# Kernel optimization log

Hardware: AMD Instinct MI355X
Metric: run time of the kernel (lower is better)

The kernel has to match this reference:

```python
import jax, jax.numpy as jnp
import numpy as np

T = 256   # time steps
F = 64    # features per step
H = 32    # LSTM hidden size
FORGET_BIAS = 1.0  # TF LSTMCell default


def setup_inputs() -> dict:
    key = jax.random.key(0)
    k1, k2, k3 = jax.random.split(key, 3)
    B = 16384
    x = jax.random.normal(k1, (B, T * F), dtype=jnp.float32)
    W_lstm = jax.random.normal(k2, (F + H, 4 * H), dtype=jnp.float32) * 0.1
    b_lstm = jnp.zeros((4 * H,), dtype=jnp.float32)
    W_dense = jax.random.normal(k3, (H, 1), dtype=jnp.float32) * 0.1
    b_dense = jnp.zeros((1,), dtype=jnp.float32)
    return {"x": x, "W_lstm": W_lstm, "b_lstm": b_lstm,
            "W_dense": W_dense, "b_dense": b_dense}


def reference(x, W_lstm, b_lstm, W_dense, b_dense):
    B = x.shape[0]
    # [B, T*F] -> [T, B, F] for scan over time
    xs = x.reshape(B, T, F).transpose(1, 0, 2)

    def step(carry, x_t):
        c, h = carry
        # TF LSTMCell: concat([inputs, h]) @ kernel + bias, gate order i, j, f, o
        gates = jnp.concatenate([x_t, h], axis=-1) @ W_lstm + b_lstm
        i, j, f, o = jnp.split(gates, 4, axis=-1)
        c_new = c * jax.nn.sigmoid(f + FORGET_BIAS) + jax.nn.sigmoid(i) * jnp.tanh(j)
        h_new = jnp.tanh(c_new) * jax.nn.sigmoid(o)
        return (c_new, h_new), None

    c0 = jnp.zeros((B, H), dtype=x.dtype)
    h0 = jnp.zeros((B, H), dtype=x.dtype)
    (c_T, h_T), _ = jax.lax.scan(step, (c0, h0), xs)

    # dense(1) + ELU on the final hidden state, then flatten like predict()
    out = jax.nn.elu(h_T @ W_dense + b_dense)
    return out.reshape(-1)
```

## Files before the change

### kernel.cpp

```cpp
#include <hip/hip_runtime.h>
#include <stdint.h>

#define T_STEPS 256
#define F_IN 64
#define L2E 1.44269504f

typedef __bf16 bf16x8 __attribute__((ext_vector_type(8)));
typedef float f32x4 __attribute__((ext_vector_type(4)));
typedef uint32_t u32;
typedef uint32_t u32x4 __attribute__((ext_vector_type(4)));

#define GLDS16(gp, lp)                                                         \
    __builtin_amdgcn_global_load_lds(                                          \
        (const __attribute__((address_space(1))) unsigned int*)(gp),           \
        (__attribute__((address_space(3))) unsigned int*)(lp), 16, 0, 0)

static __device__ __forceinline__ u32 pk2(float lo, float hi) {
    unsigned short a = __builtin_bit_cast(unsigned short, (__bf16)lo);
    unsigned short b = __builtin_bit_cast(unsigned short, (__bf16)hi);
    return (u32)a | ((u32)b << 16);
}

__global__ __launch_bounds__(256, 1)
void lstm_fused(const float* __restrict__ x,
                const float* __restrict__ Wl,
                const float* __restrict__ bl,
                const float* __restrict__ Wd,
                const float* __restrict__ bd,
                float* __restrict__ out)
{
    __shared__ __align__(16) float xs[4][4][1024];

    const int lane = threadIdx.x & 63;
    const int wid  = threadIdx.x >> 6;
    const int cl   = lane & 15;
    const int g4   = lane >> 4;
    const int rowBase = blockIdx.x * 64 + wid * 16;

#define GSC(q) (((q) >> 1) == 1 ? -2.0f * L2E : -L2E)

    bf16x8 wfrag[3][8];
#pragma unroll
    for (int kc = 0; kc < 3; ++kc) {
#pragma unroll
        for (int q = 0; q < 8; ++q) {
            bf16x8 v;
#pragma unroll
            for (int j = 0; j < 8; ++j)
                v[j] = (__bf16)(GSC(q) * Wl[(kc * 32 + g4 * 8 + j) * 128 + q * 16 + cl]);
            wfrag[kc][q] = v;
        }
    }

    f32x4 biasf[8];
#pragma unroll
    for (int q = 0; q < 8; ++q) {
#pragma unroll
        for (int r = 0; r < 4; ++r) {
            const int gate = q * 16 + g4 * 4 + r;
            biasf[q][r] = GSC(q) * (bl[gate] + ((q >> 1) == 2 ? 1.0f : 0.0f));
        }
    }
    const float bd0 = bd[0];
    float wdl[4], wdh[4];
#pragma unroll
    for (int r = 0; r < 4; ++r) {
        wdl[r] = Wd[4 * g4 + r];
        wdh[r] = Wd[16 + 4 * g4 + r];
    }

    const float* gbase = x + (size_t)(rowBase + (lane >> 2)) * (size_t)(T_STEPS * F_IN)
                           + (size_t)(((lane & 3) ^ ((lane >> 3) & 3)) * 4);

    asm volatile("s_waitcnt vmcnt(0)" ::: "memory");
    __builtin_amdgcn_sched_barrier(0);

#define STAGE(TT, SP) do {                                                     \
    const float* gp = gbase + (TT) * F_IN;                                     \
    GLDS16(gp,      &xs[wid][SP][0]);                                          \
    GLDS16(gp + 16, &xs[wid][SP][256]);                                        \
    GLDS16(gp + 32, &xs[wid][SP][512]);                                        \
    GLDS16(gp + 48, &xs[wid][SP][768]);                                        \
} while (0)

    STAGE(0, 0);
    STAGE(1, 1);
    STAGE(2, 2);

    const int swz = (cl >> 1) & 3;
    const int c0  = ((g4 & 1) * 2)     ^ swz;
    const int c1  = ((g4 & 1) * 2 + 1) ^ swz;
    const int kA  = (g4 >> 1) * 256 + cl * 16;
    const int kB  = kA + 512;

    const int srcA = cl + 32 * (g4 & 1);
    const int srcB = srcA + 16;
    const int sel  = g4 >> 1;

    f32x4 csl = {0.f, 0.f, 0.f, 0.f};
    f32x4 csh = {0.f, 0.f, 0.f, 0.f};
    f32x4 hlv, hhv;
    u32x4 ahw = {0u, 0u, 0u, 0u};
    f32x4 accx[8];

#define CELL(AI, AJ, AF, AO, CS, HV) do {                                      \
    _Pragma("unroll")                                                          \
    for (int r = 0; r < 4; ++r) {                                              \
        float I  = __builtin_amdgcn_exp2f((AI)[r]);                            \
        float J  = __builtin_amdgcn_exp2f((AJ)[r]);                            \
        float Fv = __builtin_amdgcn_exp2f((AF)[r]);                            \
        float O  = __builtin_amdgcn_exp2f((AO)[r]);                            \
        float t3 = (1.0f + I) * (1.0f + J);                                    \
        float uu = 1.0f + Fv;                                                  \
        float np = __builtin_fmaf(J, 2.0f * L2E, -2.0f * L2E);                 \
        float r1 = __builtin_amdgcn_rcpf(t3 * uu);                             \
        float nm = __builtin_fmaf((CS)[r], t3, np * uu);                       \
        float cp = nm * r1;                                                    \
        float C  = __builtin_amdgcn_exp2f(cp);                                 \
        float r2 = __builtin_amdgcn_rcpf((1.0f + C) * (1.0f + O));             \
        (HV)[r] = (1.0f - C) * r2;                                             \
        (CS)[r] = cp;                                                          \
    }                                                                          \
} while (0)

#define XGATES(SLOT) do {                                                      \
    const float* sl = &xs[wid][SLOT][0];                                       \
    f32x4 xr0 = *(const f32x4*)(sl + kA + c0 * 4);                             \
    f32x4 xr1 = *(const f32x4*)(sl + kA + c1 * 4);                             \
    f32x4 xr2 = *(const f32x4*)(sl + kB + c0 * 4);                             \
    f32x4 xr3 = *(const f32x4*)(sl + kB + c1 * 4);                             \
    bf16x8 ax0, ax1;                                                           \
    _Pragma("unroll")                                                          \
    for (int j = 0; j < 4; ++j) {                                              \
        ax0[j]     = (__bf16)xr0[j];                                           \
        ax0[4 + j] = (__bf16)xr1[j];                                           \
        ax1[j]     = (__bf16)xr2[j];                                           \
        ax1[4 + j] = (__bf16)xr3[j];                                           \
    }                                                                          \
    _Pragma("unroll")                                                          \
    for (int q = 0; q < 8; ++q) {                                              \
        f32x4 a = __builtin_amdgcn_mfma_f32_16x16x32_bf16(wfrag[0][q], ax0, biasf[q], 0, 0, 0); \
        accx[q] = __builtin_amdgcn_mfma_f32_16x16x32_bf16(wfrag[1][q], ax1, a, 0, 0, 0);        \
    }                                                                          \
} while (0)

    asm volatile("s_waitcnt vmcnt(8)" ::: "memory");
    __builtin_amdgcn_sched_barrier(0);
    XGATES(0);

#define STEP(TT) do {                                                          \
         \
    bf16x8 ah = __builtin_bit_cast(bf16x8, ahw);                               \
    f32x4 acc[8];                                                              \
    _Pragma("unroll")                                                          \
    for (int q = 0; q < 8; ++q)                                                \
        acc[q] = __builtin_amdgcn_mfma_f32_16x16x32_bf16(wfrag[2][q], ah, accx[q], 0, 0, 0); \
    CELL(acc[0], acc[2], acc[4], acc[6], csl, hlv);                            \
    CELL(acc[1], acc[3], acc[5], acc[7], csh, hhv);                            \
               \
    u32 W0 = pk2(hlv[0], hlv[1]);                                              \
    u32 W1 = pk2(hlv[2], hlv[3]);                                              \
    u32 W2 = pk2(hhv[0], hhv[1]);                                              \
    u32 W3 = pk2(hhv[2], hhv[3]);                                              \
               \
    int A0 = __shfl((int)W0, srcA, 64), A1 = __shfl((int)W1, srcA, 64);        \
    int A2 = __shfl((int)W2, srcA, 64), A3 = __shfl((int)W3, srcA, 64);        \
    int B0 = __shfl((int)W0, srcB, 64), B1 = __shfl((int)W1, srcB, 64);        \
    int B2 = __shfl((int)W2, srcB, 64), B3 = __shfl((int)W3, srcB, 64);        \
    ahw[0] = (u32)(sel ? A2 : A0);                                             \
    ahw[1] = (u32)(sel ? A3 : A1);                                             \
    ahw[2] = (u32)(sel ? B2 : B0);                                             \
    ahw[3] = (u32)(sel ? B3 : B1);                                             \
           \
    const int tpf = ((TT) + 3 < T_STEPS) ? (TT) + 3 : T_STEPS - 1;             \
    STAGE(tpf, ((TT) + 3) & 3);                                                \
    asm volatile("s_waitcnt vmcnt(8)" ::: "memory");                           \
    __builtin_amdgcn_sched_barrier(0);                                         \
    const int tn = ((TT) + 1 < T_STEPS) ? (TT) + 1 : T_STEPS - 1;              \
    XGATES(tn & 3);                                                            \
} while (0)

    for (int t = 0; t < T_STEPS; t += 4) {
        STEP(t);
        STEP(t + 1);
        STEP(t + 2);
        STEP(t + 3);
    }
#undef STEP
#undef XGATES
#undef CELL
#undef STAGE

    asm volatile("s_waitcnt vmcnt(0)" ::: "memory");

    float v = 0.f;
#pragma unroll
    for (int r = 0; r < 4; ++r) {
        v = __builtin_fmaf(hlv[r], wdl[r], v);
        v = __builtin_fmaf(hhv[r], wdh[r], v);
    }
    v += __shfl_xor(v, 16, 64);
    v += __shfl_xor(v, 32, 64);
    if (lane < 16) {
        float z = v + bd0;
        out[rowBase + lane] = z > 0.f ? z : (__expf(z) - 1.0f);
    }
}

extern "C" void kernel_launch(void* const* d_in, const int* in_sizes, int n_in,
                              void* d_out, int out_size, void* d_ws, size_t ws_size,
                              hipStream_t stream) {
    const float* x  = (const float*)d_in[0];
    const float* Wl = (const float*)d_in[1];
    const float* bl = (const float*)d_in[2];
    const float* Wd = (const float*)d_in[3];
    const float* bd = (const float*)d_in[4];
    float* out = (float*)d_out;

    const int rows = out_size;
    const int grid = (rows + 63) / 64;
    hipLaunchKernelGGL(lstm_fused, dim3(grid), dim3(256), 0, stream,
                       x, Wl, bl, Wd, bd, out);
}
```

Before: 240.1 us.

## Stage x in 4-timestep groups of contiguous 1KB row chunks with double buffering

Replaces the per-timestep prefetch, which loaded one 256-byte row slice per lane across 16 rows, with group staging. Each wave now loads 4 timesteps (1 KB contiguous) of every row with one 16-byte load per lane per row, into an XOR-swizzled LDS buffer. There are two group slots and a vmcnt wait once per 4 steps instead of every step. The aim is more contiguous global access and fewer waits per timestep, at the cost of a shallower prefetch window (one group ahead) and more load instructions issued at once.

```diff
diff --git a/kernel.cpp b/kernel.cpp
--- a/kernel.cpp
+++ b/kernel.cpp
@@ -29,7 +29,7 @@
                 const float* __restrict__ bd,
                 float* __restrict__ out)
 {
-    __shared__ __align__(16) float xs[4][4][1024];
+    __shared__ __align__(16) float xg[4][2][16][256];
 
     const int lane = threadIdx.x & 63;
     const int wid  = threadIdx.x >> 6;
@@ -69,33 +69,30 @@
         wdh[r] = Wd[16 + 4 * g4 + r];
     }
 
-    const float* gbase = x + (size_t)(rowBase + (lane >> 2)) * (size_t)(T_STEPS * F_IN)
-                           + (size_t)(((lane & 3) ^ ((lane >> 3) & 3)) * 4);
+    const char* xbase = (const char*)(x + (size_t)rowBase * (size_t)(T_STEPS * F_IN));
+    int loff[8];
+#pragma unroll
+    for (int k = 0; k < 8; ++k) loff[k] = ((lane ^ k) << 4);
 
     asm volatile("s_waitcnt vmcnt(0)" ::: "memory");
     __builtin_amdgcn_sched_barrier(0);
 
-#define STAGE(TT, SP) do {                                                     \
-    const float* gp = gbase + (TT) * F_IN;                                     \
-    GLDS16(gp,      &xs[wid][SP][0]);                                          \
-    GLDS16(gp + 16, &xs[wid][SP][256]);                                        \
-    GLDS16(gp + 32, &xs[wid][SP][512]);                                        \
-    GLDS16(gp + 48, &xs[wid][SP][768]);                                        \
-} while (0)
-
-    STAGE(0, 0);
-    STAGE(1, 1);
-    STAGE(2, 2);
-
-    const int swz = (cl >> 1) & 3;
-    const int c0  = ((g4 & 1) * 2)     ^ swz;
-    const int c1  = ((g4 & 1) * 2 + 1) ^ swz;
-    const int kA  = (g4 >> 1) * 256 + cl * 16;
-    const int kB  = kA + 512;
+#define STAGE_GROUP(G, SL) do {                                                \
+    _Pragma("unroll")                                                          \
+    for (int r = 0; r < 16; ++r) {                                             \
+        const char* gp = xbase + (size_t)r * (size_t)(T_STEPS * F_IN * 4)      \
+                       + (size_t)(G) * 1024 + loff[r & 7];                     \
+        GLDS16(gp, &xg[wid][SL][r][0]);                                        \
+    }                                                                          \
+} while (0)
+
+    STAGE_GROUP(0, 0);
+    STAGE_GROUP(1, 1);
 
     const int srcA = cl + 32 * (g4 & 1);
     const int srcB = srcA + 16;
     const int sel  = g4 >> 1;
+    const int kswz = cl & 7;
 
     f32x4 csl = {0.f, 0.f, 0.f, 0.f};
     f32x4 csh = {0.f, 0.f, 0.f, 0.f};
@@ -123,12 +120,13 @@
     }                                                                          \
 } while (0)
 
-#define XGATES(SLOT) do {                                                      \
-    const float* sl = &xs[wid][SLOT][0];                                       \
-    f32x4 xr0 = *(const f32x4*)(sl + kA + c0 * 4);                             \
-    f32x4 xr1 = *(const f32x4*)(sl + kA + c1 * 4);                             \
-    f32x4 xr2 = *(const f32x4*)(sl + kB + c0 * 4);                             \
-    f32x4 xr3 = *(const f32x4*)(sl + kB + c1 * 4);                             \
+#define XGATES(TT) do {                                                        \
+    const float* base = &xg[wid][((TT) >> 2) & 1][cl][0];                      \
+    const int c00 = (((TT) & 3) * 16 + 2 * g4) ^ kswz;                         \
+    f32x4 xr0 = *(const f32x4*)(base + (size_t)( c00          ) * 4);          \
+    f32x4 xr1 = *(const f32x4*)(base + (size_t)( c00 ^ 1      ) * 4);          \
+    f32x4 xr2 = *(const f32x4*)(base + (size_t)( c00 ^ 8      ) * 4);          \
+    f32x4 xr3 = *(const f32x4*)(base + (size_t)((c00 ^ 8) ^ 1 ) * 4);          \
     bf16x8 ax0, ax1;                                                           \
     _Pragma("unroll")                                                          \
     for (int j = 0; j < 4; ++j) {                                              \
@@ -144,12 +142,7 @@
     }                                                                          \
 } while (0)
 
-    asm volatile("s_waitcnt vmcnt(8)" ::: "memory");
-    __builtin_amdgcn_sched_barrier(0);
-    XGATES(0);
-
-#define STEP(TT) do {                                                          \
-         \
+#define CHAIN() do {                                                           \
     bf16x8 ah = __builtin_bit_cast(bf16x8, ahw);                               \
     f32x4 acc[8];                                                              \
     _Pragma("unroll")                                                          \
@@ -157,12 +150,10 @@
         acc[q] = __builtin_amdgcn_mfma_f32_16x16x32_bf16(wfrag[2][q], ah, accx[q], 0, 0, 0); \
     CELL(acc[0], acc[2], acc[4], acc[6], csl, hlv);                            \
     CELL(acc[1], acc[3], acc[5], acc[7], csh, hhv);                            \
-               \
     u32 W0 = pk2(hlv[0], hlv[1]);                                              \
     u32 W1 = pk2(hlv[2], hlv[3]);                                              \
     u32 W2 = pk2(hhv[0], hhv[1]);                                              \
     u32 W3 = pk2(hhv[2], hhv[3]);                                              \
-               \
     int A0 = __shfl((int)W0, srcA, 64), A1 = __shfl((int)W1, srcA, 64);        \
     int A2 = __shfl((int)W2, srcA, 64), A3 = __shfl((int)W3, srcA, 64);        \
     int B0 = __shfl((int)W0, srcB, 64), B1 = __shfl((int)W1, srcB, 64);        \
@@ -171,25 +162,32 @@
     ahw[1] = (u32)(sel ? A3 : A1);                                             \
     ahw[2] = (u32)(sel ? B2 : B0);                                             \
     ahw[3] = (u32)(sel ? B3 : B1);                                             \
-           \
-    const int tpf = ((TT) + 3 < T_STEPS) ? (TT) + 3 : T_STEPS - 1;             \
-    STAGE(tpf, ((TT) + 3) & 3);                                                \
-    asm volatile("s_waitcnt vmcnt(8)" ::: "memory");                           \
-    __builtin_amdgcn_sched_barrier(0);                                         \
-    const int tn = ((TT) + 1 < T_STEPS) ? (TT) + 1 : T_STEPS - 1;              \
-    XGATES(tn & 3);                                                            \
-} while (0)
-
-    for (int t = 0; t < T_STEPS; t += 4) {
-        STEP(t);
-        STEP(t + 1);
-        STEP(t + 2);
-        STEP(t + 3);
-    }
-#undef STEP
+} while (0)
+
+    asm volatile("s_waitcnt vmcnt(16)" ::: "memory");
+    __builtin_amdgcn_sched_barrier(0);
+    XGATES(0);
+
+    for (int G = 0; G < 64; ++G) {
+        const int t0 = 4 * G;
+        CHAIN(); XGATES(t0 + 1);
+        CHAIN(); XGATES(t0 + 2);
+        CHAIN(); XGATES(t0 + 3);
+        CHAIN();
+        if (G < 62) {
+            STAGE_GROUP(G + 2, G & 1);
+            asm volatile("s_waitcnt vmcnt(16)" ::: "memory");
+        } else {
+            asm volatile("s_waitcnt vmcnt(0)" ::: "memory");
+        }
+        __builtin_amdgcn_sched_barrier(0);
+        const int tn = (t0 + 4 < T_STEPS) ? t0 + 4 : T_STEPS - 1;
+        XGATES(tn);
+    }
+#undef CHAIN
 #undef XGATES
 #undef CELL
-#undef STAGE
+#undef STAGE_GROUP
 
     asm volatile("s_waitcnt vmcnt(0)" ::: "memory");
 
```

Measured after the change: 242.0 us. About the same (+0.8%).

## Halve rows per wave, double grid and occupancy, simplify staging loop

Applied to the files above, without the earlier changes.

Each wave now handles 8 batch rows instead of 16. The grid doubles and launch bounds allow two blocks per CU, which gives more waves to hide the serial recurrence latency. Shared staging shrinks to match, with a new swizzle, and the x-gate MFMAs are folded into the per-step chain with an un-unrolled loop. It also adds an s_sleep stagger for alternating groups of blocks. The risk is that half the MFMA rows are now padding (16x16 tiles with 8 real rows) and each step carries a longer MFMA dependency.

```diff
diff --git a/kernel.cpp b/kernel.cpp
--- a/kernel.cpp
+++ b/kernel.cpp
@@ -8,7 +8,6 @@
 typedef __bf16 bf16x8 __attribute__((ext_vector_type(8)));
 typedef float f32x4 __attribute__((ext_vector_type(4)));
 typedef uint32_t u32;
-typedef uint32_t u32x4 __attribute__((ext_vector_type(4)));
 
 #define GLDS16(gp, lp)                                                         \
     __builtin_amdgcn_global_load_lds(                                          \
@@ -21,7 +20,7 @@
     return (u32)a | ((u32)b << 16);
 }
 
-__global__ __launch_bounds__(256, 1)
+__global__ __launch_bounds__(256, 2)
 void lstm_fused(const float* __restrict__ x,
                 const float* __restrict__ Wl,
                 const float* __restrict__ bl,
@@ -29,13 +28,13 @@
                 const float* __restrict__ bd,
                 float* __restrict__ out)
 {
-    __shared__ __align__(16) float xs[4][4][1024];
+    __shared__ __align__(16) float xs[4][4][512];
 
     const int lane = threadIdx.x & 63;
     const int wid  = threadIdx.x >> 6;
     const int cl   = lane & 15;
     const int g4   = lane >> 4;
-    const int rowBase = blockIdx.x * 64 + wid * 16;
+    const int rowBase = blockIdx.x * 32 + wid * 8;
 
 #define GSC(q) (((q) >> 1) == 1 ? -2.0f * L2E : -L2E)
 
@@ -61,47 +60,36 @@
             biasf[q][r] = GSC(q) * (bl[gate] + ((q >> 1) == 2 ? 1.0f : 0.0f));
         }
     }
-    const float bd0 = bd[0];
-    float wdl[4], wdh[4];
-#pragma unroll
-    for (int r = 0; r < 4; ++r) {
-        wdl[r] = Wd[4 * g4 + r];
-        wdh[r] = Wd[16 + 4 * g4 + r];
-    }
 
-    const float* gbase = x + (size_t)(rowBase + (lane >> 2)) * (size_t)(T_STEPS * F_IN)
-                           + (size_t)(((lane & 3) ^ ((lane >> 3) & 3)) * 4);
+    const char* xbyte = (const char*)(x + (size_t)(rowBase + (lane >> 3)) * (size_t)(T_STEPS * F_IN))
+                      + (size_t)((((lane & 7) ^ ((lane >> 3) & 7)) << 4));
+
+    if ((blockIdx.x >> 8) & 1) __builtin_amdgcn_s_sleep(14);
 
     asm volatile("s_waitcnt vmcnt(0)" ::: "memory");
     __builtin_amdgcn_sched_barrier(0);
 
 #define STAGE(TT, SP) do {                                                     \
-    const float* gp = gbase + (TT) * F_IN;                                     \
-    GLDS16(gp,      &xs[wid][SP][0]);                                          \
-    GLDS16(gp + 16, &xs[wid][SP][256]);                                        \
-    GLDS16(gp + 32, &xs[wid][SP][512]);                                        \
-    GLDS16(gp + 48, &xs[wid][SP][768]);                                        \
+    const char* gp = xbyte + (size_t)(TT) * 256;                               \
+    GLDS16(gp,       &xs[wid][SP][0]);                                         \
+    GLDS16(gp + 128, &xs[wid][SP][256]);                                       \
 } while (0)
 
     STAGE(0, 0);
     STAGE(1, 1);
     STAGE(2, 2);
 
-    const int swz = (cl >> 1) & 3;
-    const int c0  = ((g4 & 1) * 2)     ^ swz;
-    const int c1  = ((g4 & 1) * 2 + 1) ^ swz;
-    const int kA  = (g4 >> 1) * 256 + cl * 16;
-    const int kB  = kA + 512;
-
     const int srcA = cl + 32 * (g4 & 1);
     const int srcB = srcA + 16;
     const int sel  = g4 >> 1;
+    const int r7   = cl & 7;
+    const int offA = r7 * 32 + (((2 * g4) ^ r7) << 2);
 
     f32x4 csl = {0.f, 0.f, 0.f, 0.f};
     f32x4 csh = {0.f, 0.f, 0.f, 0.f};
-    f32x4 hlv, hhv;
-    u32x4 ahw = {0u, 0u, 0u, 0u};
-    f32x4 accx[8];
+    f32x4 hlv = {0.f, 0.f, 0.f, 0.f};
+    f32x4 hhv = {0.f, 0.f, 0.f, 0.f};
+    u32 ahw0 = 0u, ahw1 = 0u, ahw2 = 0u, ahw3 = 0u;
 
 #define CELL(AI, AJ, AF, AO, CS, HV) do {                                      \
     _Pragma("unroll")                                                          \
@@ -123,71 +111,54 @@
     }                                                                          \
 } while (0)
 
-#define XGATES(SLOT) do {                                                      \
-    const float* sl = &xs[wid][SLOT][0];                                       \
-    f32x4 xr0 = *(const f32x4*)(sl + kA + c0 * 4);                             \
-    f32x4 xr1 = *(const f32x4*)(sl + kA + c1 * 4);                             \
-    f32x4 xr2 = *(const f32x4*)(sl + kB + c0 * 4);                             \
-    f32x4 xr3 = *(const f32x4*)(sl + kB + c1 * 4);                             \
-    bf16x8 ax0, ax1;                                                           \
-    _Pragma("unroll")                                                          \
-    for (int j = 0; j < 4; ++j) {                                              \
-        ax0[j]     = (__bf16)xr0[j];                                           \
-        ax0[4 + j] = (__bf16)xr1[j];                                           \
-        ax1[j]     = (__bf16)xr2[j];                                           \
-        ax1[4 + j] = (__bf16)xr3[j];                                           \
-    }                                                                          \
-    _Pragma("unroll")                                                          \
-    for (int q = 0; q < 8; ++q) {                                              \
-        f32x4 a = __builtin_amdgcn_mfma_f32_16x16x32_bf16(wfrag[0][q], ax0, biasf[q], 0, 0, 0); \
-        accx[q] = __builtin_amdgcn_mfma_f32_16x16x32_bf16(wfrag[1][q], ax1, a, 0, 0, 0);        \
-    }                                                                          \
-} while (0)
+#pragma unroll 1
+    for (int t = 0; t < T_STEPS; ++t) {
+        const int tpf = (t + 3 < T_STEPS) ? t + 3 : T_STEPS - 1;
+        STAGE(tpf, (t + 3) & 3);
+        asm volatile("s_waitcnt vmcnt(4)" ::: "memory");
+        __builtin_amdgcn_sched_barrier(0);
 
-    asm volatile("s_waitcnt vmcnt(8)" ::: "memory");
-    __builtin_amdgcn_sched_barrier(0);
-    XGATES(0);
+        const float* sl = &xs[wid][t & 3][0];
+        f32x4 xr0 = *(const f32x4*)(sl + offA);
+        f32x4 xr1 = *(const f32x4*)(sl + (offA ^ 4));
+        f32x4 xr2 = *(const f32x4*)(sl + 256 + offA);
+        f32x4 xr3 = *(const f32x4*)(sl + 256 + (offA ^ 4));
+        bf16x8 ax0, ax1;
+#pragma unroll
+        for (int j = 0; j < 4; ++j) {
+            ax0[j]     = (__bf16)xr0[j];
+            ax0[4 + j] = (__bf16)xr1[j];
+            ax1[j]     = (__bf16)xr2[j];
+            ax1[4 + j] = (__bf16)xr3[j];
+        }
 
-#define STEP(TT) do {                                                          \
-         \
-    bf16x8 ah = __builtin_bit_cast(bf16x8, ahw);                               \
-    f32x4 acc[8];                                                              \
-    _Pragma("unroll")                                                          \
-    for (int q = 0; q < 8; ++q)                                                \
-        acc[q] = __builtin_amdgcn_mfma_f32_16x16x32_bf16(wfrag[2][q], ah, accx[q], 0, 0, 0); \
-    CELL(acc[0], acc[2], acc[4], acc[6], csl, hlv);                            \
-    CELL(acc[1], acc[3], acc[5], acc[7], csh, hhv);                            \
-               \
-    u32 W0 = pk2(hlv[0], hlv[1]);                                              \
-    u32 W1 = pk2(hlv[2], hlv[3]);                                              \
-    u32 W2 = pk2(hhv[0], hhv[1]);                                              \
-    u32 W3 = pk2(hhv[2], hhv[3]);                                              \
-               \
-    int A0 = __shfl((int)W0, srcA, 64), A1 = __shfl((int)W1, srcA, 64);        \
-    int A2 = __shfl((int)W2, srcA, 64), A3 = __shfl((int)W3, srcA, 64);        \
-    int B0 = __shfl((int)W0, srcB, 64), B1 = __shfl((int)W1, srcB, 64);        \
-    int B2 = __shfl((int)W2, srcB, 64), B3 = __shfl((int)W3, srcB, 64);        \
-    ahw[0] = (u32)(sel ? A2 : A0);                                             \
-    ahw[1] = (u32)(sel ? A3 : A1);                                             \
-    ahw[2] = (u32)(sel ? B2 : B0);                                             \
-    ahw[3] = (u32)(sel ? B3 : B1);                                             \
-           \
-    const int tpf = ((TT) + 3 < T_STEPS) ? (TT) + 3 : T_STEPS - 1;             \
-    STAGE(tpf, ((TT) + 3) & 3);                                                \
-    asm volatile("s_waitcnt vmcnt(8)" ::: "memory");                           \
-    __builtin_amdgcn_sched_barrier(0);                                         \
-    const int tn = ((TT) + 1 < T_STEPS) ? (TT) + 1 : T_STEPS - 1;              \
-    XGATES(tn & 3);                                                            \
-} while (0)
+        union { u32 w[4]; bf16x8 v; } ahu;
+        ahu.w[0] = ahw0; ahu.w[1] = ahw1; ahu.w[2] = ahw2; ahu.w[3] = ahw3;
+        bf16x8 ah = ahu.v;
 
-    for (int t = 0; t < T_STEPS; t += 4) {
-        STEP(t);
-        STEP(t + 1);
-        STEP(t + 2);
-        STEP(t + 3);
+        f32x4 acc[8];
+#pragma unroll
+        for (int q = 0; q < 8; ++q) {
+            f32x4 a = __builtin_amdgcn_mfma_f32_16x16x32_bf16(wfrag[0][q], ax0, biasf[q], 0, 0, 0);
+            a = __builtin_amdgcn_mfma_f32_16x16x32_bf16(wfrag[1][q], ax1, a, 0, 0, 0);
+            acc[q] = __builtin_amdgcn_mfma_f32_16x16x32_bf16(wfrag[2][q], ah, a, 0, 0, 0);
+        }
+        CELL(acc[0], acc[2], acc[4], acc[6], csl, hlv);
+        CELL(acc[1], acc[3], acc[5], acc[7], csh, hhv);
+
+        u32 W0 = pk2(hlv[0], hlv[1]);
+        u32 W1 = pk2(hlv[2], hlv[3]);
+        u32 W2 = pk2(hhv[0], hhv[1]);
+        u32 W3 = pk2(hhv[2], hhv[3]);
+        int A0 = __shfl((int)W0, srcA, 64), A1 = __shfl((int)W1, srcA, 64);
+        int A2 = __shfl((int)W2, srcA, 64), A3 = __shfl((int)W3, srcA, 64);
+        int B0 = __shfl((int)W0, srcB, 64), B1 = __shfl((int)W1, srcB, 64);
+        int B2 = __shfl((int)W2, srcB, 64), B3 = __shfl((int)W3, srcB, 64);
+        ahw0 = (u32)(sel ? A2 : A0);
+        ahw1 = (u32)(sel ? A3 : A1);
+        ahw2 = (u32)(sel ? B2 : B0);
+        ahw3 = (u32)(sel ? B3 : B1);
     }
-#undef STEP
-#undef XGATES
 #undef CELL
 #undef STAGE
 
@@ -196,13 +167,13 @@
     float v = 0.f;
 #pragma unroll
     for (int r = 0; r < 4; ++r) {
-        v = __builtin_fmaf(hlv[r], wdl[r], v);
-        v = __builtin_fmaf(hhv[r], wdh[r], v);
+        v = __builtin_fmaf(hlv[r], Wd[4 * g4 + r], v);
+        v = __builtin_fmaf(hhv[r], Wd[16 + 4 * g4 + r], v);
     }
     v += __shfl_xor(v, 16, 64);
     v += __shfl_xor(v, 32, 64);
-    if (lane < 16) {
-        float z = v + bd0;
+    if (lane < 8) {
+        float z = v + bd[0];
         out[rowBase + lane] = z > 0.f ? z : (__expf(z) - 1.0f);
     }
 }
@@ -218,7 +189,7 @@
     float* out = (float*)d_out;
 
     const int rows = out_size;
-    const int grid = (rows + 63) / 64;
+    const int grid = (rows + 31) / 32;
     hipLaunchKernelGGL(lstm_fused, dim3(grid), dim3(256), 0, stream,
                        x, Wl, bl, Wd, bd, out);
 }
```

Result: slower. 363.1 us (+51.2%).
